# Kernel tuning notes

Hardware: AMD Instinct MI355X
Metric: run time of the kernel (lower is better)

## Reference

```python
import jax, jax.numpy as jnp
import numpy as np

B, T, L = 512, 512, 64

def setup_inputs() -> dict:
    key = jax.random.key(0)
    k1, k2, k3, k4, k5 = jax.random.split(key, 5)
    emission = jax.random.normal(k1, (B, T, L), dtype=jnp.float32)
    target = jax.random.randint(k2, (B, T), 0, L, dtype=jnp.int32)
    mask = jnp.ones((B, T), dtype=jnp.float32)
    start_trans = jax.random.uniform(k3, (L,), minval=-0.1, maxval=0.1, dtype=jnp.float32)
    trans = jax.random.uniform(k4, (L, L), minval=-0.1, maxval=0.1, dtype=jnp.float32)
    end_trans = jax.random.uniform(k5, (L,), minval=-0.1, maxval=0.1, dtype=jnp.float32)
    return {"emission": emission, "target": target, "mask": mask,
            "start_trans": start_trans, "trans": trans, "end_trans": end_trans}


def _crf_nll(emission, target, mask, start_trans, trans, end_trans):
    # end_mask: 1 at the last valid position of each sequence
    left_shift = jnp.concatenate([mask[:, 1:], jnp.zeros_like(mask[:, :1])], axis=1)
    end_mask = (mask > left_shift).astype(emission.dtype)  # [B,T]

    em_t = jnp.swapaxes(emission, 0, 1)   # [T,B,L]
    mask_t = mask.T                       # [T,B]
    endm_t = end_mask.T                   # [T,B]
    tgt_t = target.T                      # [T,B]
    brange = jnp.arange(emission.shape[0])

    # ---- normalizer: log-space forward algorithm over time ----
    init_scores = start_trans + em_t[0]   # [B,L]

    def norm_step(scores, xs):
        em_i, m_i, e_i = xs
        nxt = jax.scipy.special.logsumexp(scores[:, :, None] + trans, axis=1) + em_i
        m = m_i[:, None]
        nxt = m * nxt + (1.0 - m) * scores
        nxt = nxt + e_i[:, None] * end_trans
        return nxt, None

    scores, _ = jax.lax.scan(norm_step, init_scores, (em_t[1:], mask_t[1:], endm_t[1:]))
    normalizer = jax.scipy.special.logsumexp(scores, axis=1)  # [B]

    # ---- gold path score ----
    ps0 = start_trans[tgt_t[0]] + em_t[0][brange, tgt_t[0]]   # [B]

    def path_step(carry, xs):
        ps, prev = carry
        em_i, m_i, e_i, t_i = xs
        nxt = ps + trans[prev, t_i] + em_i[brange, t_i]
        nxt = m_i * nxt + (1.0 - m_i) * ps
        nxt = nxt + e_i * end_trans[t_i]
        return (nxt, t_i), None

    (path_scores, _), _ = jax.lax.scan(
        path_step, (ps0, tgt_t[0]), (em_t[1:], mask_t[1:], endm_t[1:], tgt_t[1:]))

    return jnp.mean(normalizer - path_scores)


def reference(emission, target, mask, start_trans, trans, end_trans):
    return _crf_nll(emission, target, mask, start_trans, trans, end_trans)
```

## Files before the change

kernel.cpp:

```cpp
#include <hip/hip_runtime.h>

#define NB 512
#define NT 512
#define NL 64
#define L2E 1.4426950408889634f
#define LN2 0.6931471805599453f

typedef _Float16 h2 __attribute__((ext_vector_type(2)));

__global__ void zero_out_kernel(float* out) { *out = 0.0f; }

__device__ __forceinline__ float dot2f(h2 a, h2 b, float c) {
#if __has_builtin(__builtin_amdgcn_fdot2)
  return __builtin_amdgcn_fdot2(a, b, c, false);
#else
  return fmaf((float)a[0], (float)b[0], fmaf((float)a[1], (float)b[1], c));
#endif
}

__device__ __forceinline__ h2 bch2(unsigned u) { return __builtin_bit_cast(h2, u); }


__device__ __forceinline__ float pairsum16(float x) {
#if __has_builtin(__builtin_amdgcn_permlane16_swap)
  unsigned xu = __float_as_uint(x);
  auto rp = __builtin_amdgcn_permlane16_swap(xu, xu, false, false);
  return __uint_as_float(rp[0]) + __uint_as_float(rp[1]);
#else
  return x + __shfl_xor(x, 16, 64);
#endif
}

__device__ __forceinline__ float pairsum32(float x) {
#if __has_builtin(__builtin_amdgcn_permlane32_swap)
  unsigned xu = __float_as_uint(x);
  auto rp = __builtin_amdgcn_permlane32_swap(xu, xu, false, false);
  return __uint_as_float(rp[0]) + __uint_as_float(rp[1]);
#else
  return x + __shfl_xor(x, 32, 64);
#endif
}


__device__ __forceinline__ float matvec64(float hval, const h2 (&ep)[4][8], int r) {
  unsigned hu = (unsigned)__builtin_bit_cast(unsigned short, (_Float16)hval);
  unsigned n1 = (unsigned)__builtin_amdgcn_mov_dpp((int)hu, 0xB1, 0xF, 0xF, true);
  unsigned p0 = hu | (n1 << 16);
  unsigned p1 = (unsigned)__builtin_amdgcn_mov_dpp((int)p0, 0x4E, 0xF, 0xF, true);
  unsigned p2 = (unsigned)__builtin_amdgcn_mov_dpp((int)p0, 0x141, 0xF, 0xF, true);
  unsigned p3 = (unsigned)__builtin_amdgcn_mov_dpp((int)p1, 0x141, 0xF, 0xF, true);
  unsigned p4 = (unsigned)__builtin_amdgcn_mov_dpp((int)p0, 0x140, 0xF, 0xF, true);
  unsigned p5 = (unsigned)__builtin_amdgcn_mov_dpp((int)p1, 0x140, 0xF, 0xF, true);
  unsigned p6 = (unsigned)__builtin_amdgcn_mov_dpp((int)p2, 0x140, 0xF, 0xF, true);
  unsigned p7 = (unsigned)__builtin_amdgcn_mov_dpp((int)p3, 0x140, 0xF, 0xF, true);
  float F[4];
#pragma unroll
  for (int q = 0; q < 4; ++q) {
    float a = dot2f(bch2(p0), ep[q][0], 0.0f);
    a = dot2f(bch2(p1), ep[q][1], a);
    a = dot2f(bch2(p2), ep[q][2], a);
    a = dot2f(bch2(p3), ep[q][3], a);
    float b = dot2f(bch2(p4), ep[q][4], 0.0f);
    b = dot2f(bch2(p5), ep[q][5], b);
    b = dot2f(bch2(p6), ep[q][6], b);
    b = dot2f(bch2(p7), ep[q][7], b);
    F[q] = pairsum32(pairsum16(a + b));
  }
  float ya = (r & 1) ? F[1] : F[0];
  float yb = (r & 1) ? F[3] : F[2];
  return (r & 2) ? yb : ya;
}

__global__
__attribute__((amdgpu_flat_work_group_size(128, 128), amdgpu_waves_per_eu(1, 1)))
void crf_nll_kernel(
    const float* __restrict__ emission,
    const int*   __restrict__ target,
    const float* __restrict__ mask,
    const float* __restrict__ start_trans,
    const float* __restrict__ trans,
    const float* __restrict__ end_trans,
    float* __restrict__ out)
{
  const int b = blockIdx.x;
  const int tid = threadIdx.x;
  const int wv = tid >> 6;
  const int j = tid & 63;
  const int r = j >> 4;
  const int c = j & 15;

  const float* em_b = emission + (size_t)b * NT * NL;
  const float* mk_b = mask + (size_t)b * NT;
  const int*   tg_b = target + (size_t)b * NT;

  __shared__ float fF[NL], fB[NL];
  __shared__ float psS[2];
  __shared__ int   GS[2];

  constexpr int PX0[8] = {0, 2, 7, 5, 15, 13, 8, 10};
  constexpr int PX1[8] = {1, 3, 6, 4, 14, 12, 9, 11};

  float ps = 0.0f;
  #pragma unroll
  for (int cc = 4 * wv; cc < 4 * wv + 4; ++cc) {
    int t = cc * 64 + j;
    int cur = tg_b[t];
    float m  = mk_b[t];
    float mn = (t + 1 < NT) ? mk_b[t + 1] : 0.0f;
    if (t == 0) {
      ps += start_trans[cur] + em_b[cur];
    } else {
      int prev = tg_b[t - 1];
      if (m > 0.5f)
        ps += trans[prev * NL + cur] + em_b[(size_t)t * NL + cur];
      if (m - mn > 0.5f)
        ps += end_trans[cur];
    }
  }
  #pragma unroll
  for (int off = 32; off; off >>= 1) ps += __shfl_down(ps, off, 64);

  const float endt = __builtin_amdgcn_exp2f(L2E * end_trans[j]);

  int G = 0;
  float s;

  if (wv == 0) {
    h2 ep[4][8];
    #pragma unroll
    for (int q = 0; q < 4; ++q) {
      const int col = 16 * q + c;
      #pragma unroll
      for (int m = 0; m < 8; ++m) {
        const int i0 = 16 * r + (c ^ PX0[m]);
        const int i1 = 16 * r + (c ^ PX1[m]);
        float e0 = __builtin_amdgcn_exp2f(L2E * trans[i0 * NL + col]);
        float e1 = __builtin_amdgcn_exp2f(L2E * trans[i1 * NL + col]);
        h2 v; v[0] = (_Float16)e0; v[1] = (_Float16)e1;
        ep[q][m] = v;
      }
    }
    s = __builtin_amdgcn_exp2f(L2E * (start_trans[j] + em_b[j]));

    float pf[8];
    #pragma unroll
    for (int u = 0; u < 8; ++u) pf[u] = L2E * em_b[(size_t)u * NL + j];

    #pragma unroll 1
    for (int cc = 0; cc < 4; ++cc) {
      const int tb = cc * 64;
      float ml = mk_b[tb + j];
      int nidx = tb + j + 1;
      float mnext = (nidx < NT) ? mk_b[nidx] : 0.0f;
      unsigned long long cm = __ballot(ml > 0.5f);
      unsigned long long ce = __ballot(ml - mnext > 0.5f);
      if (cc == 0) { cm &= ~1ull; ce &= ~1ull; }

      #pragma unroll 1
      for (int i8 = 0; i8 < 64; i8 += 8) {
        #pragma unroll
        for (int u = 0; u < 8; ++u) {
          const int i = i8 + u;
          float eemu = __builtin_amdgcn_exp2f(pf[u]);
          eemu = ((ce >> i) & 1) ? eemu * endt : eemu;
          int tp = tb + i + 8; if (tp > NT - 1) tp = NT - 1;
          pf[u] = L2E * em_b[(size_t)tp * NL + j];
          float sm = matvec64(s, ep, r);
          unsigned e0 =
            (__builtin_amdgcn_readfirstlane(__float_as_uint(sm)) >> 23) & 0xffu;
          float scale = __uint_as_float((254u - e0) << 23);
          float snew = (sm * scale) * eemu;
          float sold = s * scale;
          s = ((cm >> i) & 1) ? snew : sold;
          G += (int)e0 - 127;
        }
      }
    }
  } else {
    h2 ep[4][8];
    #pragma unroll
    for (int q = 0; q < 4; ++q) {
      const int rowi = 16 * q + c;
      #pragma unroll
      for (int m = 0; m < 8; ++m) {
        const int j0 = 16 * r + (c ^ PX0[m]);
        const int j1 = 16 * r + (c ^ PX1[m]);
        float e0 = __builtin_amdgcn_exp2f(L2E * trans[rowi * NL + j0]);
        float e1 = __builtin_amdgcn_exp2f(L2E * trans[rowi * NL + j1]);
        h2 v; v[0] = (_Float16)e0; v[1] = (_Float16)e1;
        ep[q][m] = v;
      }
    }
    s = 1.0f;

    float pf[8];
    #pragma unroll
    for (int u = 0; u < 8; ++u) pf[u] = L2E * em_b[(size_t)(504 + u) * NL + j];

    #pragma unroll 1
    for (int cc = 7; cc >= 4; --cc) {
      const int tb = cc * 64;
      float ml = mk_b[tb + j];
      int nidx = tb + j + 1;
      float mnext = (nidx < NT) ? mk_b[nidx] : 0.0f;
      unsigned long long cm = __ballot(ml > 0.5f);
      unsigned long long ce = __ballot(ml - mnext > 0.5f);

      #pragma unroll 1
      for (int i8 = 56; i8 >= 0; i8 -= 8) {
        #pragma unroll
        for (int u = 7; u >= 0; --u) {
          const int i = i8 + u;
          const int t = tb + i;
          float eemu = __builtin_amdgcn_exp2f(pf[u]);
          float wmul = ((cm >> i) & 1) ? eemu : 1.0f;
          wmul = ((ce >> i) & 1) ? wmul * endt : wmul;
          int tp = t - 8; if (tp < 0) tp = 0;
          pf[u] = L2E * em_b[(size_t)tp * NL + j];
          float w = s * wmul;
          if ((cm >> i) & 1) {
            float sm = matvec64(w, ep, r);
            unsigned e0 =
              (__builtin_amdgcn_readfirstlane(__float_as_uint(sm)) >> 23) & 0xffu;
            float scale = __uint_as_float((254u - e0) << 23);
            s = sm * scale;
            G += (int)e0 - 127;
          } else {
            s = w;
          }
        }
      }
    }
  }

  if (wv == 0) { fF[j] = s; if (j == 0) { psS[0] = ps; GS[0] = G; } }
  else         { fB[j] = s; if (j == 0) { psS[1] = ps; GS[1] = G; } }
  __syncthreads();
  if (wv == 0) {
    float prod = s * fB[j];
    #pragma unroll
    for (int off = 32; off; off >>= 1) prod += __shfl_xor(prod, off, 64);
    if (j == 0) {
      float norm = (__builtin_amdgcn_logf(prod) + (float)(GS[0] + GS[1])) * LN2;
      atomicAdd(out, (norm - psS[0] - psS[1]) * (1.0f / (float)NB));
    }
  }
}

extern "C" void kernel_launch(void* const* d_in, const int* in_sizes, int n_in,
                              void* d_out, int out_size, void* d_ws, size_t ws_size,
                              hipStream_t stream) {
  const float* emission    = (const float*)d_in[0];
  const int*   target      = (const int*)  d_in[1];
  const float* mask        = (const float*)d_in[2];
  const float* start_trans = (const float*)d_in[3];
  const float* trans       = (const float*)d_in[4];
  const float* end_trans   = (const float*)d_in[5];
  float* out = (float*)d_out;

  zero_out_kernel<<<1, 1, 0, stream>>>(out);
  crf_nll_kernel<<<NB, 128, 0, stream>>>(emission, target, mask, start_trans,
                                         trans, end_trans, out);
}
```

Measured before the change: 168.4 us.

## Switch CRF forward/backward matvec to fp32 FMA with row-rotate DPP and rescale every 4 steps

Replaces the packed fp16 dot2 matvec, which builds eight DPP-permuted half pairs, with an fp32 matvec. It uses sixteen row_ror DPP rotations and 64 fp32 FMAs per lane, with the transition exponentials stored as a float[4][16] register array. The per-step readfirstlane exponent rescale now runs only every fourth step, which shortens the serial dependency chain. This trades more VALU FMAs and registers for fewer conversions and rescales, and relies on fp32 range to absorb four unscaled steps.

```diff
diff --git a/kernel.cpp b/kernel.cpp
--- a/kernel.cpp
+++ b/kernel.cpp
@@ -6,20 +6,19 @@
 #define L2E 1.4426950408889634f
 #define LN2 0.6931471805599453f
 
-typedef _Float16 h2 __attribute__((ext_vector_type(2)));
-
 __global__ void zero_out_kernel(float* out) { *out = 0.0f; }
 
-__device__ __forceinline__ float dot2f(h2 a, h2 b, float c) {
-#if __has_builtin(__builtin_amdgcn_fdot2)
-  return __builtin_amdgcn_fdot2(a, b, c, false);
-#else
-  return fmaf((float)a[0], (float)b[0], fmaf((float)a[1], (float)b[1], c));
-#endif
-}
-
-__device__ __forceinline__ h2 bch2(unsigned u) { return __builtin_bit_cast(h2, u); }
-
+
+template <int K>
+__device__ __forceinline__ unsigned roru(unsigned x) {
+  if constexpr (K == 0) return x;
+  else
+    return (unsigned)__builtin_amdgcn_mov_dpp((int)x, 0x120 + K, 0xF, 0xF, true);
+}
+template <int K>
+__device__ __forceinline__ float rorf(float x) {
+  return __uint_as_float(roru<K>(__float_as_uint(x)));
+}
 
 __device__ __forceinline__ float pairsum16(float x) {
 #if __has_builtin(__builtin_amdgcn_permlane16_swap)
@@ -30,7 +29,6 @@
   return x + __shfl_xor(x, 16, 64);
 #endif
 }
-
 __device__ __forceinline__ float pairsum32(float x) {
 #if __has_builtin(__builtin_amdgcn_permlane32_swap)
   unsigned xu = __float_as_uint(x);
@@ -41,34 +39,39 @@
 #endif
 }
 
-
-__device__ __forceinline__ float matvec64(float hval, const h2 (&ep)[4][8], int r) {
-  unsigned hu = (unsigned)__builtin_bit_cast(unsigned short, (_Float16)hval);
-  unsigned n1 = (unsigned)__builtin_amdgcn_mov_dpp((int)hu, 0xB1, 0xF, 0xF, true);
-  unsigned p0 = hu | (n1 << 16);
-  unsigned p1 = (unsigned)__builtin_amdgcn_mov_dpp((int)p0, 0x4E, 0xF, 0xF, true);
-  unsigned p2 = (unsigned)__builtin_amdgcn_mov_dpp((int)p0, 0x141, 0xF, 0xF, true);
-  unsigned p3 = (unsigned)__builtin_amdgcn_mov_dpp((int)p1, 0x141, 0xF, 0xF, true);
-  unsigned p4 = (unsigned)__builtin_amdgcn_mov_dpp((int)p0, 0x140, 0xF, 0xF, true);
-  unsigned p5 = (unsigned)__builtin_amdgcn_mov_dpp((int)p1, 0x140, 0xF, 0xF, true);
-  unsigned p6 = (unsigned)__builtin_amdgcn_mov_dpp((int)p2, 0x140, 0xF, 0xF, true);
-  unsigned p7 = (unsigned)__builtin_amdgcn_mov_dpp((int)p3, 0x140, 0xF, 0xF, true);
-  float F[4];
-#pragma unroll
-  for (int q = 0; q < 4; ++q) {
-    float a = dot2f(bch2(p0), ep[q][0], 0.0f);
-    a = dot2f(bch2(p1), ep[q][1], a);
-    a = dot2f(bch2(p2), ep[q][2], a);
-    a = dot2f(bch2(p3), ep[q][3], a);
-    float b = dot2f(bch2(p4), ep[q][4], 0.0f);
-    b = dot2f(bch2(p5), ep[q][5], b);
-    b = dot2f(bch2(p6), ep[q][6], b);
-    b = dot2f(bch2(p7), ep[q][7], b);
-    F[q] = pairsum32(pairsum16(a + b));
-  }
-  float ya = (r & 1) ? F[1] : F[0];
-  float yb = (r & 1) ? F[3] : F[2];
+__device__ __forceinline__ float matvec64f(float s, const float (&ep)[4][16],
+                                           int r) {
+  float A0 = 0.f, A1 = 0.f, A2 = 0.f, A3 = 0.f;
+  float B0 = 0.f, B1 = 0.f, B2 = 0.f, B3 = 0.f;
+#define MAC2(K0, K1)                                   \
+  {                                                    \
+    float ta = rorf<K0>(s), tb = rorf<K1>(s);          \
+    A0 = fmaf(ta, ep[0][K0], A0);                      \
+    B0 = fmaf(tb, ep[0][K1], B0);                      \
+    A1 = fmaf(ta, ep[1][K0], A1);                      \
+    B1 = fmaf(tb, ep[1][K1], B1);                      \
+    A2 = fmaf(ta, ep[2][K0], A2);                      \
+    B2 = fmaf(tb, ep[2][K1], B2);                      \
+    A3 = fmaf(ta, ep[3][K0], A3);                      \
+    B3 = fmaf(tb, ep[3][K1], B3);                      \
+  }
+  MAC2(0, 1) MAC2(2, 3) MAC2(4, 5) MAC2(6, 7)
+  MAC2(8, 9) MAC2(10, 11) MAC2(12, 13) MAC2(14, 15)
+#undef MAC2
+  float F0 = pairsum32(pairsum16(A0 + B0));
+  float F1 = pairsum32(pairsum16(A1 + B1));
+  float F2 = pairsum32(pairsum16(A2 + B2));
+  float F3 = pairsum32(pairsum16(A3 + B3));
+  float ya = (r & 1) ? F1 : F0;
+  float yb = (r & 1) ? F3 : F2;
   return (r & 2) ? yb : ya;
+}
+
+__device__ __forceinline__ void rescale4(float& s, int& G) {
+  unsigned e0 =
+      (__builtin_amdgcn_readfirstlane(__float_as_uint(s)) >> 23) & 0xffu;
+  s *= __uint_as_float((254u - e0) << 23);
+  G += (int)e0 - 127;
 }
 
 __global__
@@ -97,8 +100,12 @@
   __shared__ float psS[2];
   __shared__ int   GS[2];
 
-  constexpr int PX0[8] = {0, 2, 7, 5, 15, 13, 8, 10};
-  constexpr int PX1[8] = {1, 3, 6, 4, 14, 12, 9, 11};
+  int pi[16];
+  pi[0] = c;
+#define PRB(K) pi[K] = (int)roru<K>((unsigned)c);
+  PRB(1) PRB(2) PRB(3) PRB(4) PRB(5) PRB(6) PRB(7) PRB(8)
+  PRB(9) PRB(10) PRB(11) PRB(12) PRB(13) PRB(14) PRB(15)
+#undef PRB
 
   float ps = 0.0f;
   #pragma unroll
@@ -126,19 +133,13 @@
   float s;
 
   if (wv == 0) {
-    h2 ep[4][8];
+    float ep[4][16];
     #pragma unroll
     for (int q = 0; q < 4; ++q) {
       const int col = 16 * q + c;
       #pragma unroll
-      for (int m = 0; m < 8; ++m) {
-        const int i0 = 16 * r + (c ^ PX0[m]);
-        const int i1 = 16 * r + (c ^ PX1[m]);
-        float e0 = __builtin_amdgcn_exp2f(L2E * trans[i0 * NL + col]);
-        float e1 = __builtin_amdgcn_exp2f(L2E * trans[i1 * NL + col]);
-        h2 v; v[0] = (_Float16)e0; v[1] = (_Float16)e1;
-        ep[q][m] = v;
-      }
+      for (int k = 0; k < 16; ++k)
+        ep[q][k] = __builtin_amdgcn_exp2f(L2E * trans[(16 * r + pi[k]) * NL + col]);
     }
     s = __builtin_amdgcn_exp2f(L2E * (start_trans[j] + em_b[j]));
 
@@ -165,31 +166,20 @@
           eemu = ((ce >> i) & 1) ? eemu * endt : eemu;
           int tp = tb + i + 8; if (tp > NT - 1) tp = NT - 1;
           pf[u] = L2E * em_b[(size_t)tp * NL + j];
-          float sm = matvec64(s, ep, r);
-          unsigned e0 =
-            (__builtin_amdgcn_readfirstlane(__float_as_uint(sm)) >> 23) & 0xffu;
-          float scale = __uint_as_float((254u - e0) << 23);
-          float snew = (sm * scale) * eemu;
-          float sold = s * scale;
-          s = ((cm >> i) & 1) ? snew : sold;
-          G += (int)e0 - 127;
+          float sm = matvec64f(s, ep, r) * eemu;
+          s = ((cm >> i) & 1) ? sm : s;
+          if ((u & 3) == 3) rescale4(s, G);
         }
       }
     }
   } else {
-    h2 ep[4][8];
+    float ep[4][16];
     #pragma unroll
     for (int q = 0; q < 4; ++q) {
       const int rowi = 16 * q + c;
       #pragma unroll
-      for (int m = 0; m < 8; ++m) {
-        const int j0 = 16 * r + (c ^ PX0[m]);
-        const int j1 = 16 * r + (c ^ PX1[m]);
-        float e0 = __builtin_amdgcn_exp2f(L2E * trans[rowi * NL + j0]);
-        float e1 = __builtin_amdgcn_exp2f(L2E * trans[rowi * NL + j1]);
-        h2 v; v[0] = (_Float16)e0; v[1] = (_Float16)e1;
-        ep[q][m] = v;
-      }
+      for (int k = 0; k < 16; ++k)
+        ep[q][k] = __builtin_amdgcn_exp2f(L2E * trans[rowi * NL + 16 * r + pi[k]]);
     }
     s = 1.0f;
 
@@ -218,16 +208,9 @@
           int tp = t - 8; if (tp < 0) tp = 0;
           pf[u] = L2E * em_b[(size_t)tp * NL + j];
           float w = s * wmul;
-          if ((cm >> i) & 1) {
-            float sm = matvec64(w, ep, r);
-            unsigned e0 =
-              (__builtin_amdgcn_readfirstlane(__float_as_uint(sm)) >> 23) & 0xffu;
-            float scale = __uint_as_float((254u - e0) << 23);
-            s = sm * scale;
-            G += (int)e0 - 127;
-          } else {
-            s = w;
-          }
+          if ((cm >> i) & 1) s = matvec64f(w, ep, r);
+          else               s = w;
+          if ((u & 3) == 0) rescale4(s, G);
         }
       }
     }
```

After: 174.3 us. 3.5% more time.
